# Kernel optimization log

Hardware: AMD Instinct MI355X
Metric: run time of the kernel (lower is better)

Reference implementation:

```python
import jax, jax.numpy as jnp
import numpy as np

LATENT_DIM = 8
POLY_DEGREE = 5
DATA_DIM = 64
BATCH = 4096
TOTAL_TERMS = sum(LATENT_DIM ** d for d in range(POLY_DEGREE + 1))  # 37449


def _poly_features(z):
    # z: [B, L] -> [B, sum_d L^d] concatenated Kronecker powers, degree 0..D.
    B = z.shape[0]
    feats = [jnp.ones((B, 1), dtype=z.dtype)]  # degree 0
    cur = z  # degree 1: [B, L]
    feats.append(cur)
    for _ in range(2, POLY_DEGREE + 1):
        # kron(cur, z) per sample: outer product then flatten (row-major matches torch.kron)
        cur = (cur[:, :, None] * z[:, None, :]).reshape(B, -1)
        feats.append(cur)
    return jnp.concatenate(feats, axis=1)  # [B, TOTAL_TERMS]


def setup_inputs() -> dict:
    key = jax.random.key(0)
    k1, k2, k3 = jax.random.split(key, 3)
    z = jax.random.normal(k1, (BATCH, LATENT_DIM), dtype=jnp.float32)
    W = jax.random.normal(k2, (DATA_DIM, TOTAL_TERMS), dtype=jnp.float32) / np.sqrt(TOTAL_TERMS)
    b = jax.random.normal(k3, (DATA_DIM,), dtype=jnp.float32)
    return {"z": z, "W": W, "b": b}


def reference(z, W, b):
    feats = _poly_features(z)                 # [B, TOTAL_TERMS]
    return feats @ W.T + b                    # [B, DATA_DIM]
```

## Files before the change

### kernel.cpp

```cpp
#include <hip/hip_runtime.h>


#define TOTAL_TERMS 37449
#define NSTEP 1172
#define MBLK 32
#define KY 16
#define OUT_ELEMS 262144

typedef _Float16 half8 __attribute__((ext_vector_type(8)));
typedef float f32x4 __attribute__((ext_vector_type(4)));

__global__ __launch_bounds__(256) void convert_w(const float* __restrict__ W,
                                                 const float* __restrict__ bias,
                                                 _Float16* __restrict__ Wt) {
    __shared__ _Float16 lds[64][72];
    int tid  = threadIdx.x;
    int lane = tid & 63;
    int nq   = tid >> 6;
    int kb   = blockIdx.x * 64;
    int kp   = kb + lane;

    int o, mode;
    if (kp < 8)           { o = 1 + kp;            mode = 0; }
    else if (kp == 8)     { o = 0;                 mode = 2; }
    else if (kp < 32)     { o = 0;                 mode = 1; }
    else if (kp < 96)     { o = 9    + (kp - 32);  mode = 0; }
    else if (kp < 608)    { o = 73   + (kp - 96);  mode = 0; }
    else if (kp < 4704)   { o = 585  + (kp - 608); mode = 0; }
    else if (kp < 37472)  { o = 4681 + (kp - 4704);mode = 0; }
    else                  { o = 0;                 mode = 1; }

#pragma unroll
    for (int r = 0; r < 16; ++r) {
        int n = r * 4 + nq;
        const float* wrow = W + (size_t)n * TOTAL_TERMS;
        float v;
        if (mode == 1)      v = 0.f;
        else if (mode == 2) v = wrow[0] + bias[n];
        else                v = wrow[o];
        lds[n][lane] = (_Float16)v;
    }
    __syncthreads();

    int quad = lane >> 4, l16 = lane & 15;
    int n = nq * 16 + l16;
#pragma unroll
    for (int sl = 0; sl < 2; ++sl) {
        int kk = sl * 32 + quad * 8;
        half8 hv;
#pragma unroll
        for (int j = 0; j < 8; ++j) hv[j] = lds[n][kk + j];
        int s = (kb >> 5) + sl;
        *(half8*)(Wt + ((size_t)(s * 4 + nq) * 64 + lane) * 8) = hv;
    }
}

__global__ __launch_bounds__(256, 2) void poly_gemm(const float* __restrict__ z,
                                                    const _Float16* __restrict__ Wt,
                                                    float* __restrict__ part,
                                                    float* __restrict__ out,
                                                    int use_atomic) {
    __shared__ __align__(16) _Float16 zm[128][8];
    __shared__ _Float16 zT[8][144];

    int tid  = threadIdx.x;
    int lane = tid & 63;
    int w    = tid >> 6;
    int g    = w >> 1;
    int h    = w & 1;
    int mb   = blockIdx.x;
    int ky   = blockIdx.y;

    const char* gb  = (const char*)Wt + (size_t)((147 + 64 * ky) * 4 + 2 * h) * 1024
                    + (size_t)lane * 16;
    const char* gb4 = (const char*)Wt + (size_t)((19 + 8 * ky) * 4 + 2 * h) * 1024
                    + (size_t)lane * 16;

    half8 Bk[2][16];
#pragma unroll
    for (int ii = 0; ii < 8; ++ii)
#pragma unroll
        for (int k = 0; k < 2; ++k)
            Bk[0][ii * 2 + k] = *(const half8*)(gb + ii * 4096 + k * 1024);

    if (tid < 128) {
        const float* zp = z + ((size_t)(mb * 128 + tid)) * 8;
        float4 a = *(const float4*)zp;
        float4 b4 = *(const float4*)(zp + 4);
        half8 hz;
        hz[0] = (_Float16)a.x;  hz[1] = (_Float16)a.y;
        hz[2] = (_Float16)a.z;  hz[3] = (_Float16)a.w;
        hz[4] = (_Float16)b4.x; hz[5] = (_Float16)b4.y;
        hz[6] = (_Float16)b4.z; hz[7] = (_Float16)b4.w;
        *(half8*)&zm[tid][0] = hz;
#pragma unroll
        for (int j = 0; j < 8; ++j) zT[j][tid] = hz[j];
    }
    __syncthreads();

    int quad = lane >> 4;
    int l16  = lane & 15;
    int mrow[4];
    half8 zv[4];
    _Float16 zq[4], zq4[4];
#pragma unroll
    for (int t = 0; t < 4; ++t) {
        mrow[t] = g * 64 + t * 16 + l16;
        zv[t]   = *(const half8*)&zm[mrow[t]][0];
        zq[t]   = zT[quad][mrow[t]];
        zq4[t]  = zT[quad + 4][mrow[t]];
    }

    f32x4 acc[4][2];
#pragma unroll
    for (int t = 0; t < 4; ++t)
#pragma unroll
        for (int k = 0; k < 2; ++k) acc[t][k] = (f32x4){0.f, 0.f, 0.f, 0.f};

    _Float16 a1[4];
#pragma unroll
    for (int t = 0; t < 4; ++t) a1[t] = zT[ky >> 1][mrow[t]];

    for (int sc = 0; sc < 4; ++sc) {
        int rtop = (4 * ky + sc) & 7;
        _Float16 gz[4];
#pragma unroll
        for (int t = 0; t < 4; ++t) gz[t] = a1[t] * zT[rtop][mrow[t]];
#pragma unroll
        for (int gp = 0; gp < 2; ++gp) {
            const char* gn = (sc == 3 && gp == 1) ? gb4 : (gb + 32768);
#pragma unroll
            for (int ii = 0; ii < 8; ++ii)
#pragma unroll
                for (int k = 0; k < 2; ++k)
                    Bk[gp ^ 1][ii * 2 + k] =
                        *(const half8*)(gn + ii * 4096 + k * 1024);
#pragma unroll
            for (int ii = 0; ii < 8; ++ii) {
                const int r3 = gp * 4 + (ii >> 1);
                half8 av[4];
#pragma unroll
                for (int t = 0; t < 4; ++t) {
                    _Float16 f = gz[t] * zv[t][r3] *
                                 ((ii & 1) ? zq4[t] : zq[t]);
                    av[t] = zv[t] * f;
                }
#pragma unroll
                for (int t = 0; t < 4; ++t)
#pragma unroll
                    for (int k = 0; k < 2; ++k)
                        acc[t][k] = __builtin_amdgcn_mfma_f32_16x16x32_f16(
                            av[t], Bk[gp][ii * 2 + k], acc[t][k], 0, 0, 0);
            }
            gb += 32768;
        }
    }

    {
        const char* ge0 = (const char*)Wt + (size_t)(ky * 4 + 2 * h) * 1024
                        + (size_t)lane * 16;
        Bk[1][0] = *(const half8*)(ge0);
        Bk[1][1] = *(const half8*)(ge0 + 1024);
        if (ky < 3) {
            const char* ge1 = (const char*)Wt
                            + (size_t)((16 + ky) * 4 + 2 * h) * 1024
                            + (size_t)lane * 16;
            Bk[1][2] = *(const half8*)(ge1);
            Bk[1][3] = *(const half8*)(ge1 + 1024);
        }
        const int r3b = (ky & 1) * 4;
        _Float16 d2z[4][4];
#pragma unroll
        for (int j = 0; j < 4; ++j)
#pragma unroll
            for (int t = 0; t < 4; ++t) d2z[t][j] = zT[r3b + j][mrow[t]];
#pragma unroll
        for (int ii = 0; ii < 8; ++ii) {
            half8 av[4];
#pragma unroll
            for (int t = 0; t < 4; ++t) {
                _Float16 f = a1[t] * d2z[t][ii >> 1] *
                             ((ii & 1) ? zq4[t] : zq[t]);
                av[t] = zv[t] * f;
            }
#pragma unroll
            for (int t = 0; t < 4; ++t)
#pragma unroll
                for (int k = 0; k < 2; ++k)
                    acc[t][k] = __builtin_amdgcn_mfma_f32_16x16x32_f16(
                        av[t], Bk[0][ii * 2 + k], acc[t][k], 0, 0, 0);
        }
    }

    {
        half8 av[4];
        if (ky == 0) {
#pragma unroll
            for (int t = 0; t < 4; ++t) {
                if (quad == 0)      av[t] = zv[t];
                else if (quad == 1) { av[t] = (half8){}; av[t][0] = (_Float16)1.f; }
                else                av[t] = (half8){};
            }
        } else if (ky < 3) {
            int r1 = (ky - 1) * 4 + quad;
#pragma unroll
            for (int t = 0; t < 4; ++t) {
                _Float16 f = zT[r1][mrow[t]];
                av[t] = zv[t] * f;
            }
        } else {
            int u = ky - 3;
            int r1 = u >> 1, r2 = ((u & 1) << 2) + quad;
#pragma unroll
            for (int t = 0; t < 4; ++t) {
                _Float16 f = zT[r1][mrow[t]] * zT[r2][mrow[t]];
                av[t] = zv[t] * f;
            }
        }
#pragma unroll
        for (int t = 0; t < 4; ++t)
#pragma unroll
            for (int k = 0; k < 2; ++k)
                acc[t][k] = __builtin_amdgcn_mfma_f32_16x16x32_f16(
                    av[t], Bk[1][k], acc[t][k], 0, 0, 0);

        if (ky < 3) {
            int u = 13 + ky;
            int r1 = u >> 1, r2 = ((u & 1) << 2) + quad;
#pragma unroll
            for (int t = 0; t < 4; ++t) {
                _Float16 f = zT[r1][mrow[t]] * zT[r2][mrow[t]];
                av[t] = zv[t] * f;
            }
#pragma unroll
            for (int t = 0; t < 4; ++t)
#pragma unroll
                for (int k = 0; k < 2; ++k)
                    acc[t][k] = __builtin_amdgcn_mfma_f32_16x16x32_f16(
                        av[t], Bk[1][2 + k], acc[t][k], 0, 0, 0);
        }
    }

    float* dstbase = use_atomic ? out : (part + (size_t)ky * OUT_ELEMS);
#pragma unroll
    for (int t = 0; t < 4; ++t) {
        int mbase = mb * 128 + g * 64 + t * 16 + quad * 4;
#pragma unroll
        for (int k = 0; k < 2; ++k) {
            int col = h * 32 + k * 16 + l16;
#pragma unroll
            for (int r = 0; r < 4; ++r) {
                size_t idx = (size_t)(mbase + r) * 64 + col;
                if (use_atomic) unsafeAtomicAdd(out + idx, acc[t][k][r]);
                else __builtin_nontemporal_store(acc[t][k][r], dstbase + idx);
            }
        }
    }
}

__global__ __launch_bounds__(256) void reduce_part(const float* __restrict__ part,
                                                   float* __restrict__ out) {
    int gid = blockIdx.x * 256 + threadIdx.x;
    const f32x4* p4 = (const f32x4*)part;
    f32x4 s = (f32x4){0.f, 0.f, 0.f, 0.f};
#pragma unroll
    for (int j = 0; j < KY; ++j)
        s += __builtin_nontemporal_load(p4 + (size_t)j * (OUT_ELEMS / 4) + gid);
    __builtin_nontemporal_store(s, ((f32x4*)out) + gid);
}

extern "C" void kernel_launch(void* const* d_in, const int* in_sizes, int n_in,
                              void* d_out, int out_size, void* d_ws, size_t ws_size,
                              hipStream_t stream) {
    (void)in_sizes; (void)n_in;
    const float* z = (const float*)d_in[0];
    const float* W = (const float*)d_in[1];
    const float* b = (const float*)d_in[2];
    float* out = (float*)d_out;

    const size_t part_bytes = (size_t)KY * OUT_ELEMS * sizeof(float);
    const size_t wt_bytes   = (size_t)(NSTEP + 16) * 2048 * sizeof(_Float16);
    const bool two_phase = ws_size >= part_bytes + wt_bytes;

    float* part;
    _Float16* Wt;
    if (two_phase) {
        part = (float*)d_ws;
        Wt   = (_Float16*)((char*)d_ws + part_bytes);
    } else {
        part = out;
        Wt   = (_Float16*)d_ws;
    }

    if (!two_phase)
        hipMemsetAsync(d_out, 0, (size_t)out_size * sizeof(float), stream);
    hipLaunchKernelGGL(convert_w, dim3(NSTEP / 2), dim3(256), 0, stream, W, b, Wt);
    hipLaunchKernelGGL(poly_gemm, dim3(MBLK, KY), dim3(256), 0, stream,
                       z, Wt, part, out, two_phase ? 0 : 1);
    if (two_phase)
        hipLaunchKernelGGL(reduce_part, dim3(OUT_ELEMS / 4 / 256), dim3(256), 0,
                           stream, part, out);
}
```

Measured before the change: 93.58 us.

## Fuse weight conversion, GEMM, and reduction into one persistent kernel with grid barriers

Merges the three kernel launches (weight fp16 conversion, split-K GEMM, partial-sum reduction) into a single 512-block kernel that uses a global atomic-counter grid barrier between phases. This removes two launch gaps and inter-kernel drain overhead. It relies on all 512 blocks being co-resident (two per CU at launch bounds 256,2) and adds spin-wait barrier latency. The larger shared-memory footprint of the fused kernel could reduce occupancy.

```diff
diff --git a/kernel.cpp b/kernel.cpp
--- a/kernel.cpp
+++ b/kernel.cpp
@@ -6,18 +6,38 @@
 #define MBLK 32
 #define KY 16
 #define OUT_ELEMS 262144
+#define GRID 512
 
 typedef _Float16 half8 __attribute__((ext_vector_type(8)));
 typedef float f32x4 __attribute__((ext_vector_type(4)));
 
-__global__ __launch_bounds__(256) void convert_w(const float* __restrict__ W,
-                                                 const float* __restrict__ bias,
-                                                 _Float16* __restrict__ Wt) {
-    __shared__ _Float16 lds[64][72];
-    int tid  = threadIdx.x;
+__device__ unsigned long long g_bar;
+
+__device__ __forceinline__ void grid_barrier(int tid) {
+    __syncthreads();
+    if (tid == 0) {
+        __threadfence();
+        unsigned long long v = atomicAdd(&g_bar, 1ull);
+        unsigned long long target = (v / GRID + 1) * GRID;
+        long long spins = 0;
+        while (__hip_atomic_load(&g_bar, __ATOMIC_RELAXED,
+                                 __HIP_MEMORY_SCOPE_AGENT) < target) {
+            __builtin_amdgcn_s_sleep(2);
+            if (++spins > (1ll << 27)) break;
+        }
+        __threadfence();
+    }
+    __syncthreads();
+}
+
+__device__ __forceinline__ void convert_tile(const float* __restrict__ W,
+                                             const float* __restrict__ bias,
+                                             _Float16* __restrict__ Wt,
+                                             _Float16 (*lds)[72],
+                                             int tb, int tid) {
     int lane = tid & 63;
     int nq   = tid >> 6;
-    int kb   = blockIdx.x * 64;
+    int kb   = tb * 64;
     int kp   = kb + lane;
 
     int o, mode;
@@ -50,26 +70,24 @@
         half8 hv;
 #pragma unroll
         for (int j = 0; j < 8; ++j) hv[j] = lds[n][kk + j];
-        int s = (kb >> 5) + sl;
+        int s = tb * 2 + sl;
         *(half8*)(Wt + ((size_t)(s * 4 + nq) * 64 + lane) * 8) = hv;
     }
-}
-
-__global__ __launch_bounds__(256, 2) void poly_gemm(const float* __restrict__ z,
-                                                    const _Float16* __restrict__ Wt,
-                                                    float* __restrict__ part,
-                                                    float* __restrict__ out,
-                                                    int use_atomic) {
-    __shared__ __align__(16) _Float16 zm[128][8];
-    __shared__ _Float16 zT[8][144];
-
-    int tid  = threadIdx.x;
+    __syncthreads();
+}
+
+__device__ __forceinline__ void gemm_body(const float* __restrict__ z,
+                                          const _Float16* __restrict__ Wt,
+                                          float* __restrict__ part,
+                                          float* __restrict__ out,
+                                          int use_atomic, int mb, int ky,
+                                          int tid,
+                                          _Float16 (*zm)[8],
+                                          _Float16 (*zT)[144]) {
     int lane = tid & 63;
     int w    = tid >> 6;
     int g    = w >> 1;
     int h    = w & 1;
-    int mb   = blockIdx.x;
-    int ky   = blockIdx.y;
 
     const char* gb  = (const char*)Wt + (size_t)((147 + 64 * ky) * 4 + 2 * h) * 1024
                     + (size_t)lane * 16;
@@ -258,15 +276,55 @@
     }
 }
 
-__global__ __launch_bounds__(256) void reduce_part(const float* __restrict__ part,
-                                                   float* __restrict__ out) {
-    int gid = blockIdx.x * 256 + threadIdx.x;
-    const f32x4* p4 = (const f32x4*)part;
-    f32x4 s = (f32x4){0.f, 0.f, 0.f, 0.f};
-#pragma unroll
-    for (int j = 0; j < KY; ++j)
-        s += __builtin_nontemporal_load(p4 + (size_t)j * (OUT_ELEMS / 4) + gid);
-    __builtin_nontemporal_store(s, ((f32x4*)out) + gid);
+__global__ __launch_bounds__(256, 2) void poly_fused(const float* __restrict__ z,
+                                                     const float* __restrict__ W,
+                                                     const float* __restrict__ bias,
+                                                     _Float16* __restrict__ Wt,
+                                                     float* __restrict__ part,
+                                                     float* __restrict__ out) {
+    __shared__ _Float16 clds[64][72];
+    __shared__ __align__(16) _Float16 zm[128][8];
+    __shared__ _Float16 zT[8][144];
+
+    int tid = threadIdx.x;
+    int bid = blockIdx.x;
+
+    for (int tb = bid; tb < NSTEP / 2; tb += GRID)
+        convert_tile(W, bias, Wt, clds, tb, tid);
+
+    grid_barrier(tid);
+
+    gemm_body(z, Wt, part, out, 0, bid >> 4, bid & 15, tid, zm, zT);
+
+    grid_barrier(tid);
+
+    int gid = bid * 256 + tid;
+    if (gid < OUT_ELEMS / 4) {
+        const f32x4* p4 = (const f32x4*)part;
+        f32x4 s = (f32x4){0.f, 0.f, 0.f, 0.f};
+#pragma unroll
+        for (int j = 0; j < KY; ++j)
+            s += __builtin_nontemporal_load(p4 + (size_t)j * (OUT_ELEMS / 4) + gid);
+        __builtin_nontemporal_store(s, ((f32x4*)out) + gid);
+    }
+}
+
+__global__ __launch_bounds__(256) void convert_w(const float* __restrict__ W,
+                                                 const float* __restrict__ bias,
+                                                 _Float16* __restrict__ Wt) {
+    __shared__ _Float16 lds[64][72];
+    convert_tile(W, bias, Wt, lds, blockIdx.x, threadIdx.x);
+}
+
+__global__ __launch_bounds__(256, 2) void poly_gemm(const float* __restrict__ z,
+                                                    const _Float16* __restrict__ Wt,
+                                                    float* __restrict__ part,
+                                                    float* __restrict__ out,
+                                                    int use_atomic) {
+    __shared__ __align__(16) _Float16 zm[128][8];
+    __shared__ _Float16 zT[8][144];
+    gemm_body(z, Wt, part, out, use_atomic, blockIdx.x, blockIdx.y,
+              threadIdx.x, zm, zT);
 }
 
 extern "C" void kernel_launch(void* const* d_in, const int* in_sizes, int n_in,
@@ -282,22 +340,17 @@
     const size_t wt_bytes   = (size_t)(NSTEP + 16) * 2048 * sizeof(_Float16);
     const bool two_phase = ws_size >= part_bytes + wt_bytes;
 
-    float* part;
-    _Float16* Wt;
     if (two_phase) {
-        part = (float*)d_ws;
-        Wt   = (_Float16*)((char*)d_ws + part_bytes);
+        float* part = (float*)d_ws;
+        _Float16* Wt = (_Float16*)((char*)d_ws + part_bytes);
+        hipLaunchKernelGGL(poly_fused, dim3(GRID), dim3(256), 0, stream,
+                           z, W, b, Wt, part, out);
     } else {
-        part = out;
-        Wt   = (_Float16*)d_ws;
-    }
-
-    if (!two_phase)
+        _Float16* Wt = (_Float16*)d_ws;
         hipMemsetAsync(d_out, 0, (size_t)out_size * sizeof(float), stream);
-    hipLaunchKernelGGL(convert_w, dim3(NSTEP / 2), dim3(256), 0, stream, W, b, Wt);
-    hipLaunchKernelGGL(poly_gemm, dim3(MBLK, KY), dim3(256), 0, stream,
-                       z, Wt, part, out, two_phase ? 0 : 1);
-    if (two_phase)
-        hipLaunchKernelGGL(reduce_part, dim3(OUT_ELEMS / 4 / 256), dim3(256), 0,
-                           stream, part, out);
-}
+        hipLaunchKernelGGL(convert_w, dim3(NSTEP / 2), dim3(256), 0, stream,
+                           W, b, Wt);
+        hipLaunchKernelGGL(poly_gemm, dim3(MBLK, KY), dim3(256), 0, stream,
+                           z, Wt, out, out, 1);
+    }
+}
```

After: 195.7 us. 109% more time.
